# Optimization experiments

Measured on AMD Instinct MI355X. Metric: run time of the kernel, lower is better.

The kernel has to match this reference:

```python
import jax, jax.numpy as jnp
import numpy as np


def setup_inputs() -> dict:
    key = jax.random.key(0)
    k1, k2 = jax.random.split(key)
    B, T, D = 16, 512, 384
    x = jax.random.normal(k1, (B, T, D), dtype=jnp.float32)
    durations = jax.random.randint(k2, (B, T), 0, 16, dtype=jnp.int32)
    return {"x": x, "durations": durations, "target_len": 4096}


def reference(x, durations, target_len):
    # x: [B, T, D] phoneme embeddings; durations: [B, T] frame counts.
    # Original clamps each duration to at least 1 via max(1, int(d)).
    dur = jnp.maximum(durations, 1)                      # [B, T]
    cum = jnp.cumsum(dur, axis=1)                        # [B, T] exclusive end positions
    total = cum[:, -1]                                   # [B] per-sequence frame count
    t = jnp.arange(target_len, dtype=cum.dtype)          # [L]
    # For output frame t, source phoneme = first i with cum[i] > t.
    idx = jax.vmap(lambda c: jnp.searchsorted(c, t, side='right'))(cum)  # [B, L]
    idx = jnp.minimum(idx, x.shape[1] - 1)
    out = jnp.take_along_axis(x, idx[..., None], axis=1)  # [B, L, D]
    # Frames past the expanded length are zero padding.
    valid = (t[None, :] < total[:, None])[..., None]       # [B, L, 1]
    return jnp.where(valid, out, jnp.zeros((), dtype=x.dtype))
```

## Files before the change

### kernel.cpp

```cpp
#include <hip/hip_runtime.h>

#define B_   16
#define T_   512
#define TLEN 4096
#define XC   96
#define RPB  16
#define SENT 0xFFFFu

typedef float f4v __attribute__((ext_vector_type(4)));

__device__ __forceinline__ int sniff_dur(const unsigned int* __restrict__ durw,
                                         int e) {
    int f32ok = 1, i64ok = 1, i32ok = 1, i16ok = 1;
    #pragma unroll
    for (int k = 0; k < 32; ++k) {
        unsigned w = durw[k];
        f32ok &= (int)((w == 0u) | ((w >= 0x3F800000u) & (w <= 0x41700000u)));
        i64ok &= (int)((k & 1) ? (w == 0u) : (w <= 15u));
        i32ok &= (int)(w <= 15u);
        i16ok &= (int)(((w & 0xFFFFu) <= 15u) & ((w >> 16) <= 15u));
    }
    int v;
    if (f32ok)      v = (int)__uint_as_float(durw[e]);
    else if (i64ok) v = (int)durw[e * 2];
    else if (i32ok) v = (int)durw[e];
    else if (i16ok) v = (int)((durw[e >> 1] >> (16 * (e & 1))) & 0xFFFFu);
    else            v = (int)durw[e];
    return v;
}

__global__ __launch_bounds__(T_) void lr_build_idx(const unsigned int* __restrict__ durw,
                                                   unsigned short* __restrict__ idx) {
    __shared__ int s[T_];
    const int b = blockIdx.x;
    const int t = threadIdx.x;

    int v = sniff_dur(durw, b * T_ + t);
    s[t] = v < 1 ? 1 : v;
    __syncthreads();
    for (int off = 1; off < T_; off <<= 1) {
        int add = (t >= off) ? s[t - off] : 0;
        __syncthreads();
        s[t] += add;
        __syncthreads();
    }
    const int cum  = s[t];
    const int prev = t ? s[t - 1] : 0;

    unsigned short* row = idx + b * TLEN;
    for (int i = t; i < TLEN; i += T_) row[i] = (unsigned short)SENT;
    __syncthreads();

    const int end = cum < TLEN ? cum : TLEN;
    for (int j = prev; j < end; ++j) row[j] = (unsigned short)t;
}

__global__ __launch_bounds__(384) void lr_expand_idx(const f4v* __restrict__ x,
                                                     const unsigned short* __restrict__ idx,
                                                     f4v* __restrict__ out) {
    const int tid = threadIdx.x;
    const int sub = tid / XC;
    const int col = tid - sub * XC;
    const int row0 = blockIdx.x * RPB + sub;
    const int b = (blockIdx.x * RPB) >> 12;

    unsigned iv[4];
    #pragma unroll
    for (int p = 0; p < 4; ++p) iv[p] = idx[row0 + p * 4];

    f4v v[4];
    #pragma unroll
    for (int p = 0; p < 4; ++p) {
        v[p] = (f4v){0.f, 0.f, 0.f, 0.f};
        if (iv[p] != SENT) v[p] = x[(b * T_ + (int)iv[p]) * XC + col];
    }

    #pragma unroll
    for (int p = 0; p < 4; ++p)
        out[(size_t)(row0 + p * 4) * XC + col] = v[p];
}

__global__ __launch_bounds__(T_) void lr_scan(const unsigned int* __restrict__ durw,
                                              int* __restrict__ cum) {
    __shared__ int s[T_];
    const int b = blockIdx.x;
    const int t = threadIdx.x;
    int v = sniff_dur(durw, b * T_ + t);
    s[t] = v < 1 ? 1 : v;
    __syncthreads();
    for (int off = 1; off < T_; off <<= 1) {
        int add = (t >= off) ? s[t - off] : 0;
        __syncthreads();
        s[t] += add;
        __syncthreads();
    }
    cum[b * T_ + t] = s[t];
}

__global__ __launch_bounds__(384) void lr_expand(const f4v* __restrict__ x,
                                                 const int* __restrict__ cum,
                                                 f4v* __restrict__ out) {
    __shared__ int sc[T_];
    const int tid  = threadIdx.x;
    const int row0 = blockIdx.x * 32;
    const int b    = row0 >> 12;
    for (int i = tid; i < T_; i += 384) sc[i] = cum[b * T_ + i];
    __syncthreads();
    const int total = sc[T_ - 1];
    const int sub = tid / XC;
    const int col = tid - sub * XC;
    #pragma unroll
    for (int p = 0; p < 8; ++p) {
        const int row = row0 + p * 4 + sub;
        const int t   = row & (TLEN - 1);
        f4v val = (f4v){0.f, 0.f, 0.f, 0.f};
        if (t < total) {
            int lo = 0, hi = T_;
            #pragma unroll
            for (int i = 0; i < 10; ++i) {
                int mid = (lo + hi) >> 1;
                if (sc[mid] > t) hi = mid; else lo = mid + 1;
            }
            const int idx2 = lo > (T_ - 1) ? (T_ - 1) : lo;
            val = x[(b * T_ + idx2) * XC + col];
        }
        out[(size_t)row * XC + col] = val;
    }
}

extern "C" void kernel_launch(void* const* d_in, const int* in_sizes, int n_in,
                              void* d_out, int out_size, void* d_ws, size_t ws_size,
                              hipStream_t stream) {
    const f4v* x = (const f4v*)d_in[0];
    const unsigned int* durw = (const unsigned int*)d_in[1];

    if (ws_size >= (size_t)(B_ * TLEN * 2)) {
        unsigned short* idx = (unsigned short*)d_ws;
        lr_build_idx<<<B_, T_, 0, stream>>>(durw, idx);
        lr_expand_idx<<<(B_ * TLEN) / RPB, 384, 0, stream>>>(x, idx, (f4v*)d_out);
    } else {
        int* cum = (int*)d_ws;
        lr_scan<<<B_, T_, 0, stream>>>(durw, cum);
        lr_expand<<<(B_ * TLEN) / 32, 384, 0, stream>>>(x, cum, (f4v*)d_out);
    }
}
```

Before: 125.5 us.

## Fuse duration scan and expansion into a single kernel with per-block scan

Replaces the two-kernel path (build index table in workspace, then gather) with one kernel where every block recomputes the 512-element prefix sum of its batch's durations in shared memory, then binary-searches each output row and gathers from x. This removes a kernel launch, the serial dependency between kernels, and the index-table writes and reads. In exchange each of 4096 blocks redoes the scan (9 barrier rounds, duration loads) and a 10-step shared-memory binary search per row, adding per-block latency.

```diff
diff --git a/kernel.cpp b/kernel.cpp
--- a/kernel.cpp
+++ b/kernel.cpp
@@ -5,7 +5,7 @@
 #define TLEN 4096
 #define XC   96
 #define RPB  16
-#define SENT 0xFFFFu
+#define NTHR 384
 
 typedef float f4v __attribute__((ext_vector_type(4)));
 
@@ -29,50 +29,56 @@
     return v;
 }
 
-__global__ __launch_bounds__(T_) void lr_build_idx(const unsigned int* __restrict__ durw,
-                                                   unsigned short* __restrict__ idx) {
+__global__ __launch_bounds__(NTHR) void lr_fused(const f4v* __restrict__ x,
+                                                 const unsigned int* __restrict__ durw,
+                                                 f4v* __restrict__ out) {
     __shared__ int s[T_];
-    const int b = blockIdx.x;
-    const int t = threadIdx.x;
+    const int tid  = threadIdx.x;
+    const int base = blockIdx.x * RPB;
+    const int b    = base >> 12;
 
-    int v = sniff_dur(durw, b * T_ + t);
-    s[t] = v < 1 ? 1 : v;
-    __syncthreads();
-    for (int off = 1; off < T_; off <<= 1) {
-        int add = (t >= off) ? s[t - off] : 0;
+    {
+        const int i0 = tid, i1 = tid + NTHR;
+        int v0 = sniff_dur(durw, b * T_ + i0);
+        s[i0] = v0 < 1 ? 1 : v0;
+        if (i1 < T_) {
+            int v1 = sniff_dur(durw, b * T_ + i1);
+            s[i1] = v1 < 1 ? 1 : v1;
+        }
         __syncthreads();
-        s[t] += add;
-        __syncthreads();
+        for (int off = 1; off < T_; off <<= 1) {
+            int a0 = (i0 >= off) ? s[i0 - off] : 0;
+            int a1 = (i1 < T_) ? s[i1 - off] : 0;
+            __syncthreads();
+            s[i0] += a0;
+            if (i1 < T_) s[i1] += a1;
+            __syncthreads();
+        }
     }
-    const int cum  = s[t];
-    const int prev = t ? s[t - 1] : 0;
+    const int total = s[T_ - 1];
 
-    unsigned short* row = idx + b * TLEN;
-    for (int i = t; i < TLEN; i += T_) row[i] = (unsigned short)SENT;
-    __syncthreads();
+    const int sub  = tid / XC;
+    const int col  = tid - sub * XC;
+    const int row0 = base + sub;
 
-    const int end = cum < TLEN ? cum : TLEN;
-    for (int j = prev; j < end; ++j) row[j] = (unsigned short)t;
-}
-
-__global__ __launch_bounds__(384) void lr_expand_idx(const f4v* __restrict__ x,
-                                                     const unsigned short* __restrict__ idx,
-                                                     f4v* __restrict__ out) {
-    const int tid = threadIdx.x;
-    const int sub = tid / XC;
-    const int col = tid - sub * XC;
-    const int row0 = blockIdx.x * RPB + sub;
-    const int b = (blockIdx.x * RPB) >> 12;
-
-    unsigned iv[4];
+    int ix[4];
     #pragma unroll
-    for (int p = 0; p < 4; ++p) iv[p] = idx[row0 + p * 4];
+    for (int p = 0; p < 4; ++p) {
+        const int t = (row0 + p * 4) & (TLEN - 1);
+        int lo = 0, hi = T_;
+        #pragma unroll
+        for (int k = 0; k < 10; ++k) {
+            int mid = (lo + hi) >> 1;
+            if (s[mid] > t) hi = mid; else lo = mid + 1;
+        }
+        ix[p] = (t < total) ? (lo > (T_ - 1) ? (T_ - 1) : lo) : -1;
+    }
 
     f4v v[4];
     #pragma unroll
     for (int p = 0; p < 4; ++p) {
         v[p] = (f4v){0.f, 0.f, 0.f, 0.f};
-        if (iv[p] != SENT) v[p] = x[(b * T_ + (int)iv[p]) * XC + col];
+        if (ix[p] >= 0) v[p] = x[(b * T_ + ix[p]) * XC + col];
     }
 
     #pragma unroll
@@ -80,67 +86,12 @@
         out[(size_t)(row0 + p * 4) * XC + col] = v[p];
 }
 
-__global__ __launch_bounds__(T_) void lr_scan(const unsigned int* __restrict__ durw,
-                                              int* __restrict__ cum) {
-    __shared__ int s[T_];
-    const int b = blockIdx.x;
-    const int t = threadIdx.x;
-    int v = sniff_dur(durw, b * T_ + t);
-    s[t] = v < 1 ? 1 : v;
-    __syncthreads();
-    for (int off = 1; off < T_; off <<= 1) {
-        int add = (t >= off) ? s[t - off] : 0;
-        __syncthreads();
-        s[t] += add;
-        __syncthreads();
-    }
-    cum[b * T_ + t] = s[t];
-}
-
-__global__ __launch_bounds__(384) void lr_expand(const f4v* __restrict__ x,
-                                                 const int* __restrict__ cum,
-                                                 f4v* __restrict__ out) {
-    __shared__ int sc[T_];
-    const int tid  = threadIdx.x;
-    const int row0 = blockIdx.x * 32;
-    const int b    = row0 >> 12;
-    for (int i = tid; i < T_; i += 384) sc[i] = cum[b * T_ + i];
-    __syncthreads();
-    const int total = sc[T_ - 1];
-    const int sub = tid / XC;
-    const int col = tid - sub * XC;
-    #pragma unroll
-    for (int p = 0; p < 8; ++p) {
-        const int row = row0 + p * 4 + sub;
-        const int t   = row & (TLEN - 1);
-        f4v val = (f4v){0.f, 0.f, 0.f, 0.f};
-        if (t < total) {
-            int lo = 0, hi = T_;
-            #pragma unroll
-            for (int i = 0; i < 10; ++i) {
-                int mid = (lo + hi) >> 1;
-                if (sc[mid] > t) hi = mid; else lo = mid + 1;
-            }
-            const int idx2 = lo > (T_ - 1) ? (T_ - 1) : lo;
-            val = x[(b * T_ + idx2) * XC + col];
-        }
-        out[(size_t)row * XC + col] = val;
-    }
-}
-
 extern "C" void kernel_launch(void* const* d_in, const int* in_sizes, int n_in,
                               void* d_out, int out_size, void* d_ws, size_t ws_size,
                               hipStream_t stream) {
     const f4v* x = (const f4v*)d_in[0];
     const unsigned int* durw = (const unsigned int*)d_in[1];
+    (void)d_ws; (void)ws_size;
 
-    if (ws_size >= (size_t)(B_ * TLEN * 2)) {
-        unsigned short* idx = (unsigned short*)d_ws;
-        lr_build_idx<<<B_, T_, 0, stream>>>(durw, idx);
-        lr_expand_idx<<<(B_ * TLEN) / RPB, 384, 0, stream>>>(x, idx, (f4v*)d_out);
-    } else {
-        int* cum = (int*)d_ws;
-        lr_scan<<<B_, T_, 0, stream>>>(durw, cum);
-        lr_expand<<<(B_ * TLEN) / 32, 384, 0, stream>>>(x, cum, (f4v*)d_out);
-    }
+    lr_fused<<<(B_ * TLEN) / RPB, NTHR, 0, stream>>>(x, durw, (f4v*)d_out);
 }
```

Measured after the change: 142.6 us. 13.6% more time.
